# Kernel tuning notes

Hardware: AMD Instinct MI355X
Metric: run time of the kernel (lower is better)

Reference implementation:

```python
import jax, jax.numpy as jnp
import numpy as np

B, S, D_IN, D_OUT, RANK = 4, 2048, 4096, 4096, 16
SCALING = 32.0 / RANK  # alpha / rank
MASK_DENSITY = 0.01


def setup_inputs() -> dict:
    key = jax.random.key(0)
    ks = jax.random.split(key, 7)
    x = jax.random.normal(ks[0], (B, S, D_IN), dtype=jnp.float32)
    W = jax.random.normal(ks[1], (D_OUT, D_IN), dtype=jnp.float32) / np.sqrt(D_IN)
    b = jax.random.normal(ks[2], (D_OUT,), dtype=jnp.float32) * 0.01
    lora_A = jax.random.normal(ks[3], (RANK, D_IN), dtype=jnp.float32) / np.sqrt(D_IN)
    lora_B = jax.random.normal(ks[4], (D_OUT, RANK), dtype=jnp.float32) * 0.01
    delta = jax.random.normal(ks[5], (D_OUT, D_IN), dtype=jnp.float32) * 0.01
    mask = jax.random.bernoulli(ks[6], MASK_DENSITY, (D_OUT, D_IN))
    return {"x": x, "W": W, "b": b, "lora_A": lora_A, "lora_B": lora_B,
            "delta": delta, "mask": mask}


def reference(x, W, b, lora_A, lora_B, delta, mask):
    # frozen linear: [B,S,D_in] @ [D_in,D_out] + b
    out = jnp.einsum("bsd,od->bso", x, W) + b
    # LoRA branch: (x @ A^T) @ B^T * scaling
    out = out + jnp.einsum("bsr,or->bso", jnp.einsum("bsd,rd->bsr", x, lora_A), lora_B) * SCALING
    # sparse delta branch: F.linear(x, delta * mask)
    masked_delta = delta * mask.astype(delta.dtype)
    out = out + jnp.einsum("bsd,od->bso", x, masked_delta)
    return out
```

## Files before the change

### kernel.cpp

```cpp
#include <hip/hip_runtime.h>
#include <hip/hip_bf16.h>

typedef __hip_bfloat16 bf16;
typedef __attribute__((ext_vector_type(8))) short bf16x8;
typedef __attribute__((ext_vector_type(4))) float f32x4;
typedef __attribute__((ext_vector_type(4))) int int4v;

#define AS1 __attribute__((address_space(1)))
#define AS3 __attribute__((address_space(3)))

#define MDIM 8192
#define NDIM 4096
#define KDIM 4096
#define SCALING 2.0f

__device__ int g_isf32;

static __device__ __forceinline__ float tofl(bf16 v)  { return __bfloat162float(v); }
static __device__ __forceinline__ float tofl(float v) { return v; }

static __device__ __forceinline__ void load8(const bf16* p, float* o) {
    bf16x8 v = *(const bf16x8*)p;
    const bf16* b = (const bf16*)&v;
#pragma unroll
    for (int e = 0; e < 8; ++e) o[e] = __bfloat162float(b[e]);
}
static __device__ __forceinline__ void load8(const float* p, float* o) {
    f32x4 a = *(const f32x4*)p;
    f32x4 c = *(const f32x4*)(p + 4);
#pragma unroll
    for (int e = 0; e < 4; ++e) { o[e] = a[e]; o[e + 4] = c[e]; }
}

__global__ __launch_bounds__(256) void detect_dtype(const unsigned short* xw) {
    __shared__ int cnt;
    if (threadIdx.x == 0) cnt = 0;
    __syncthreads();
    int local = 0;
    for (int i = threadIdx.x; i < 16384; i += 256) {
        unsigned v = xw[i];
        if (((v >> 7) & 0xFFu) == 0xFFu) local++;
    }
    if (local) atomicAdd(&cnt, local);
    __syncthreads();
    if (threadIdx.x == 0) g_isf32 = (cnt > 0) ? 1 : 0;
}

template <typename TIN>
__global__ __launch_bounds__(256) void fold_weff(
    const TIN* __restrict__ W, const TIN* __restrict__ lA,
    const TIN* __restrict__ lB, const TIN* __restrict__ delta,
    const int* __restrict__ mask, bf16* __restrict__ Weff, int want)
{
    if (g_isf32 != want) return;
    int idx = blockIdx.x * 256 + threadIdx.x;
    int o   = idx >> 9;
    int d0  = (idx & 511) << 3;
    size_t base = (size_t)o * KDIM + d0;

    float Bo[16];
#pragma unroll
    for (int r = 0; r < 16; ++r) Bo[r] = tofl(lB[o * 16 + r]);

    float wv[8], dv[8];
    load8(W + base, wv);
    load8(delta + base, dv);

    int mk[8];
    *(int4v*)(mk)     = *(const int4v*)(mask + base);
    *(int4v*)(mk + 4) = *(const int4v*)(mask + base + 4);

    float lor[8] = {0.f, 0.f, 0.f, 0.f, 0.f, 0.f, 0.f, 0.f};
#pragma unroll
    for (int r = 0; r < 16; ++r) {
        float av[8];
        load8(lA + (size_t)r * KDIM + d0, av);
#pragma unroll
        for (int e = 0; e < 8; ++e) lor[e] += Bo[r] * av[e];
    }

    int4v ov4;
    bf16* ov = (bf16*)&ov4;
#pragma unroll
    for (int e = 0; e < 8; ++e) {
        float a = wv[e] + SCALING * lor[e];
        if (mk[e]) a += dv[e];
        ov[e] = __float2bfloat16(a);
    }
    *(int4v*)(Weff + base) = ov4;
}

__global__ __launch_bounds__(256, 3) void gemm_bf16(
    const bf16* __restrict__ X, const bf16* __restrict__ Wt,
    const bf16* __restrict__ bias, bf16* __restrict__ out)
{
    if (g_isf32 != 0) return;
    __shared__ bf16 As[128 * 64];
    __shared__ bf16 Bs[128 * 64];

    const int tid  = threadIdx.x;
    const int lane = tid & 63;
    const int wave = tid >> 6;
    const int wm   = wave & 1;
    const int wn   = wave >> 1;
    const int quad = lane >> 4;
    const int l16  = lane & 15;

    const int bn = blockIdx.x * 128;
    const int bm = blockIdx.y * 128;
    const int cwave = tid & ~63;

    f32x4 acc[4][4];
#pragma unroll
    for (int i = 0; i < 4; ++i)
#pragma unroll
        for (int j = 0; j < 4; ++j)
            acc[i][j] = (f32x4){0.f, 0.f, 0.f, 0.f};

    for (int kt = 0; kt < KDIM / 64; ++kt) {
        const int k0 = kt * 64;
        if (kt) __syncthreads();
#pragma unroll
        for (int j = 0; j < 4; ++j) {
            const int c  = j * 256 + tid;
            const int m  = c >> 3;
            const int kc = (c & 7) ^ (m & 7);
            const int cb = j * 256 + cwave;
            __builtin_amdgcn_global_load_lds(
                (const AS1 void*)(X + (size_t)(bm + m) * KDIM + k0 + kc * 8),
                (AS3 void*)(As + cb * 8), 16, 0, 0);
            __builtin_amdgcn_global_load_lds(
                (const AS1 void*)(Wt + (size_t)(bn + m) * KDIM + k0 + kc * 8),
                (AS3 void*)(Bs + cb * 8), 16, 0, 0);
        }
        __syncthreads();

#pragma unroll
        for (int ks = 0; ks < 2; ++ks) {
            bf16x8 af[4], bfr[4];
#pragma unroll
            for (int i = 0; i < 4; ++i) {
                const int m   = wm * 64 + i * 16 + l16;
                const int kca = (ks * 4 + quad) ^ (m & 7);
                af[i] = *(const bf16x8*)(As + m * 64 + kca * 8);
                const int n   = wn * 64 + i * 16 + l16;
                const int kcb = (ks * 4 + quad) ^ (n & 7);
                bfr[i] = *(const bf16x8*)(Bs + n * 64 + kcb * 8);
            }
#pragma unroll
            for (int i = 0; i < 4; ++i)
#pragma unroll
                for (int j = 0; j < 4; ++j)
                    acc[i][j] = __builtin_amdgcn_mfma_f32_16x16x32_bf16(
                        af[i], bfr[j], acc[i][j], 0, 0, 0);
        }
    }

    float bv[4];
#pragma unroll
    for (int j = 0; j < 4; ++j)
        bv[j] = tofl(bias[bn + wn * 64 + j * 16 + l16]);

#pragma unroll
    for (int i = 0; i < 4; ++i) {
        const int mg = bm + wm * 64 + i * 16 + quad * 4;
#pragma unroll
        for (int j = 0; j < 4; ++j) {
            const int ng = bn + wn * 64 + j * 16 + l16;
#pragma unroll
            for (int r = 0; r < 4; ++r)
                out[(size_t)(mg + r) * NDIM + ng] =
                    __float2bfloat16(acc[i][j][r] + bv[j]);
        }
    }
}

__global__ __launch_bounds__(256, 3) void gemm_f32(
    const float* __restrict__ X, const bf16* __restrict__ Wt,
    const float* __restrict__ bias, float* __restrict__ out)
{
    if (g_isf32 != 1) return;
    __shared__ float Asf[128 * 64];
    __shared__ bf16  Bs[128 * 64];

    const int tid  = threadIdx.x;
    const int lane = tid & 63;
    const int wave = tid >> 6;
    const int wm   = wave & 1;
    const int wn   = wave >> 1;
    const int quad = lane >> 4;
    const int l16  = lane & 15;

    const int bn = blockIdx.x * 128;
    const int bm = blockIdx.y * 128;
    const int cwave = tid & ~63;

    f32x4 acc[4][4];
#pragma unroll
    for (int i = 0; i < 4; ++i)
#pragma unroll
        for (int j = 0; j < 4; ++j)
            acc[i][j] = (f32x4){0.f, 0.f, 0.f, 0.f};

    for (int kt = 0; kt < KDIM / 64; ++kt) {
        const int k0 = kt * 64;
        if (kt) __syncthreads();

#pragma unroll
        for (int j = 0; j < 8; ++j) {
            const int c  = j * 256 + tid;
            const int m  = c >> 4;
            const int kc = (c & 15) ^ (m & 15);
            const int cb = j * 256 + cwave;
            __builtin_amdgcn_global_load_lds(
                (const AS1 void*)(X + (size_t)(bm + m) * KDIM + k0 + kc * 4),
                (AS3 void*)(Asf + cb * 4), 16, 0, 0);
        }
#pragma unroll
        for (int j = 0; j < 4; ++j) {
            const int c  = j * 256 + tid;
            const int m  = c >> 3;
            const int kc = (c & 7) ^ (m & 7);
            const int cb = j * 256 + cwave;
            __builtin_amdgcn_global_load_lds(
                (const AS1 void*)(Wt + (size_t)(bn + m) * KDIM + k0 + kc * 8),
                (AS3 void*)(Bs + cb * 8), 16, 0, 0);
        }
        __syncthreads();

#pragma unroll
        for (int ks = 0; ks < 2; ++ks) {
            bf16x8 af[4], bfr[4];
#pragma unroll
            for (int i = 0; i < 4; ++i) {
                const int m  = wm * 64 + i * 16 + l16;
                const int k2 = (ks * 4 + quad) * 2;
                f32x4 lo = *(const f32x4*)(Asf + m * 64 + ((k2     ^ (m & 15)) * 4));
                f32x4 hi = *(const f32x4*)(Asf + m * 64 + (((k2+1) ^ (m & 15)) * 4));
                bf16 tmp[8];
#pragma unroll
                for (int e = 0; e < 4; ++e) {
                    tmp[e]     = __float2bfloat16(lo[e]);
                    tmp[e + 4] = __float2bfloat16(hi[e]);
                }
                af[i] = *(const bf16x8*)tmp;

                const int n   = wn * 64 + i * 16 + l16;
                const int kcb = (ks * 4 + quad) ^ (n & 7);
                bfr[i] = *(const bf16x8*)(Bs + n * 64 + kcb * 8);
            }
#pragma unroll
            for (int i = 0; i < 4; ++i)
#pragma unroll
                for (int j = 0; j < 4; ++j)
                    acc[i][j] = __builtin_amdgcn_mfma_f32_16x16x32_bf16(
                        af[i], bfr[j], acc[i][j], 0, 0, 0);
        }
    }

    float bv[4];
#pragma unroll
    for (int j = 0; j < 4; ++j)
        bv[j] = bias[bn + wn * 64 + j * 16 + l16];

#pragma unroll
    for (int i = 0; i < 4; ++i) {
        const int mg = bm + wm * 64 + i * 16 + quad * 4;
#pragma unroll
        for (int j = 0; j < 4; ++j) {
            const int ng = bn + wn * 64 + j * 16 + l16;
#pragma unroll
            for (int r = 0; r < 4; ++r)
                out[(size_t)(mg + r) * NDIM + ng] = acc[i][j][r] + bv[j];
        }
    }
}

extern "C" void kernel_launch(void* const* d_in, const int* in_sizes, int n_in,
                              void* d_out, int out_size, void* d_ws, size_t ws_size,
                              hipStream_t stream)
{
    bf16* Weff = (bf16*)d_ws;

    detect_dtype<<<1, 256, 0, stream>>>((const unsigned short*)d_in[0]);

    fold_weff<float><<<dim3((NDIM * KDIM / 8) / 256), 256, 0, stream>>>(
        (const float*)d_in[1], (const float*)d_in[3], (const float*)d_in[4],
        (const float*)d_in[5], (const int*)d_in[6], Weff, 1);
    gemm_f32<<<dim3(NDIM / 128, MDIM / 128), 256, 0, stream>>>(
        (const float*)d_in[0], Weff, (const float*)d_in[2], (float*)d_out);

    fold_weff<bf16><<<dim3((NDIM * KDIM / 8) / 256), 256, 0, stream>>>(
        (const bf16*)d_in[1], (const bf16*)d_in[3], (const bf16*)d_in[4],
        (const bf16*)d_in[5], (const int*)d_in[6], Weff, 0);
    gemm_bf16<<<dim3(NDIM / 128, MDIM / 128), 256, 0, stream>>>(
        (const bf16*)d_in[0], Weff, (const bf16*)d_in[2], (bf16*)d_out);
}
```

Baseline: 728.8 us.

## Pre-convert activations to bf16 and use bf16 GEMM, drop dtype detection

Removes the runtime dtype-detection kernel and the duplicate no-op launches, specialising every path for float32 inputs. When workspace allows, x is converted to bf16 in a separate pass so the GEMM loads half the bytes per A tile, uses a smaller LDS footprint and can raise occupancy (launch bounds 4). This costs an extra read/write pass over x and needs a larger workspace, otherwise it falls back to the mixed f32/bf16 GEMM.

```diff
diff --git a/kernel.cpp b/kernel.cpp
--- a/kernel.cpp
+++ b/kernel.cpp
@@ -14,45 +14,11 @@
 #define KDIM 4096
 #define SCALING 2.0f
 
-__device__ int g_isf32;
-
-static __device__ __forceinline__ float tofl(bf16 v)  { return __bfloat162float(v); }
-static __device__ __forceinline__ float tofl(float v) { return v; }
-
-static __device__ __forceinline__ void load8(const bf16* p, float* o) {
-    bf16x8 v = *(const bf16x8*)p;
-    const bf16* b = (const bf16*)&v;
-#pragma unroll
-    for (int e = 0; e < 8; ++e) o[e] = __bfloat162float(b[e]);
-}
-static __device__ __forceinline__ void load8(const float* p, float* o) {
-    f32x4 a = *(const f32x4*)p;
-    f32x4 c = *(const f32x4*)(p + 4);
-#pragma unroll
-    for (int e = 0; e < 4; ++e) { o[e] = a[e]; o[e + 4] = c[e]; }
-}
-
-__global__ __launch_bounds__(256) void detect_dtype(const unsigned short* xw) {
-    __shared__ int cnt;
-    if (threadIdx.x == 0) cnt = 0;
-    __syncthreads();
-    int local = 0;
-    for (int i = threadIdx.x; i < 16384; i += 256) {
-        unsigned v = xw[i];
-        if (((v >> 7) & 0xFFu) == 0xFFu) local++;
-    }
-    if (local) atomicAdd(&cnt, local);
-    __syncthreads();
-    if (threadIdx.x == 0) g_isf32 = (cnt > 0) ? 1 : 0;
-}
-
-template <typename TIN>
 __global__ __launch_bounds__(256) void fold_weff(
-    const TIN* __restrict__ W, const TIN* __restrict__ lA,
-    const TIN* __restrict__ lB, const TIN* __restrict__ delta,
-    const int* __restrict__ mask, bf16* __restrict__ Weff, int want)
-{
-    if (g_isf32 != want) return;
+    const float* __restrict__ W, const float* __restrict__ lA,
+    const float* __restrict__ lB, const float* __restrict__ delta,
+    const int* __restrict__ mask, bf16* __restrict__ Weff)
+{
     int idx = blockIdx.x * 256 + threadIdx.x;
     int o   = idx >> 9;
     int d0  = (idx & 511) << 3;
@@ -60,11 +26,12 @@
 
     float Bo[16];
 #pragma unroll
-    for (int r = 0; r < 16; ++r) Bo[r] = tofl(lB[o * 16 + r]);
-
-    float wv[8], dv[8];
-    load8(W + base, wv);
-    load8(delta + base, dv);
+    for (int r = 0; r < 16; ++r) Bo[r] = lB[o * 16 + r];
+
+    f32x4 wa = *(const f32x4*)(W + base);
+    f32x4 wb = *(const f32x4*)(W + base + 4);
+    f32x4 da = *(const f32x4*)(delta + base);
+    f32x4 db = *(const f32x4*)(delta + base + 4);
 
     int mk[8];
     *(int4v*)(mk)     = *(const int4v*)(mask + base);
@@ -73,28 +40,48 @@
     float lor[8] = {0.f, 0.f, 0.f, 0.f, 0.f, 0.f, 0.f, 0.f};
 #pragma unroll
     for (int r = 0; r < 16; ++r) {
-        float av[8];
-        load8(lA + (size_t)r * KDIM + d0, av);
-#pragma unroll
-        for (int e = 0; e < 8; ++e) lor[e] += Bo[r] * av[e];
+        f32x4 aa = *(const f32x4*)(lA + (size_t)r * KDIM + d0);
+        f32x4 ab = *(const f32x4*)(lA + (size_t)r * KDIM + d0 + 4);
+#pragma unroll
+        for (int e = 0; e < 4; ++e) {
+            lor[e]     += Bo[r] * aa[e];
+            lor[e + 4] += Bo[r] * ab[e];
+        }
     }
 
     int4v ov4;
     bf16* ov = (bf16*)&ov4;
 #pragma unroll
     for (int e = 0; e < 8; ++e) {
-        float a = wv[e] + SCALING * lor[e];
-        if (mk[e]) a += dv[e];
+        float w = (e < 4) ? wa[e] : wb[e - 4];
+        float d = (e < 4) ? da[e] : db[e - 4];
+        float a = w + SCALING * lor[e];
+        if (mk[e]) a += d;
         ov[e] = __float2bfloat16(a);
     }
     *(int4v*)(Weff + base) = ov4;
 }
 
-__global__ __launch_bounds__(256, 3) void gemm_bf16(
+__global__ __launch_bounds__(256) void convert_x(
+    const float* __restrict__ X, bf16* __restrict__ Xb)
+{
+    size_t i = ((size_t)blockIdx.x * 256 + threadIdx.x) * 8;
+    f32x4 a = *(const f32x4*)(X + i);
+    f32x4 b = *(const f32x4*)(X + i + 4);
+    int4v ov4;
+    bf16* ov = (bf16*)&ov4;
+#pragma unroll
+    for (int e = 0; e < 4; ++e) {
+        ov[e]     = __float2bfloat16(a[e]);
+        ov[e + 4] = __float2bfloat16(b[e]);
+    }
+    *(int4v*)(Xb + i) = ov4;
+}
+
+__global__ __launch_bounds__(256, 4) void gemm_bf16(
     const bf16* __restrict__ X, const bf16* __restrict__ Wt,
-    const bf16* __restrict__ bias, bf16* __restrict__ out)
-{
-    if (g_isf32 != 0) return;
+    const float* __restrict__ bias, float* __restrict__ out)
+{
     __shared__ bf16 As[128 * 64];
     __shared__ bf16 Bs[128 * 64];
 
@@ -159,7 +146,7 @@
     float bv[4];
 #pragma unroll
     for (int j = 0; j < 4; ++j)
-        bv[j] = tofl(bias[bn + wn * 64 + j * 16 + l16]);
+        bv[j] = bias[bn + wn * 64 + j * 16 + l16];
 
 #pragma unroll
     for (int i = 0; i < 4; ++i) {
@@ -169,8 +156,7 @@
             const int ng = bn + wn * 64 + j * 16 + l16;
 #pragma unroll
             for (int r = 0; r < 4; ++r)
-                out[(size_t)(mg + r) * NDIM + ng] =
-                    __float2bfloat16(acc[i][j][r] + bv[j]);
+                out[(size_t)(mg + r) * NDIM + ng] = acc[i][j][r] + bv[j];
         }
     }
 }
@@ -179,7 +165,6 @@
     const float* __restrict__ X, const bf16* __restrict__ Wt,
     const float* __restrict__ bias, float* __restrict__ out)
 {
-    if (g_isf32 != 1) return;
     __shared__ float Asf[128 * 64];
     __shared__ bf16  Bs[128 * 64];
 
@@ -205,7 +190,6 @@
     for (int kt = 0; kt < KDIM / 64; ++kt) {
         const int k0 = kt * 64;
         if (kt) __syncthreads();
-
 #pragma unroll
         for (int j = 0; j < 8; ++j) {
             const int c  = j * 256 + tid;
@@ -280,19 +264,29 @@
                               void* d_out, int out_size, void* d_ws, size_t ws_size,
                               hipStream_t stream)
 {
+    const float* x     = (const float*)d_in[0];
+    const float* W     = (const float*)d_in[1];
+    const float* b     = (const float*)d_in[2];
+    const float* lA    = (const float*)d_in[3];
+    const float* lB    = (const float*)d_in[4];
+    const float* delta = (const float*)d_in[5];
+    const int*   mask  = (const int*)d_in[6];
+    float* out = (float*)d_out;
+
     bf16* Weff = (bf16*)d_ws;
-
-    detect_dtype<<<1, 256, 0, stream>>>((const unsigned short*)d_in[0]);
-
-    fold_weff<float><<<dim3((NDIM * KDIM / 8) / 256), 256, 0, stream>>>(
-        (const float*)d_in[1], (const float*)d_in[3], (const float*)d_in[4],
-        (const float*)d_in[5], (const int*)d_in[6], Weff, 1);
-    gemm_f32<<<dim3(NDIM / 128, MDIM / 128), 256, 0, stream>>>(
-        (const float*)d_in[0], Weff, (const float*)d_in[2], (float*)d_out);
-
-    fold_weff<bf16><<<dim3((NDIM * KDIM / 8) / 256), 256, 0, stream>>>(
-        (const bf16*)d_in[1], (const bf16*)d_in[3], (const bf16*)d_in[4],
-        (const bf16*)d_in[5], (const int*)d_in[6], Weff, 0);
-    gemm_bf16<<<dim3(NDIM / 128, MDIM / 128), 256, 0, stream>>>(
-        (const bf16*)d_in[0], Weff, (const bf16*)d_in[2], (bf16*)d_out);
-}
+    bf16* Xb   = (bf16*)((char*)d_ws + (size_t)NDIM * KDIM * 2);
+
+    const size_t need = (size_t)NDIM * KDIM * 2 + (size_t)MDIM * KDIM * 2;
+
+    fold_weff<<<dim3((NDIM * KDIM / 8) / 256), 256, 0, stream>>>(
+        W, lA, lB, delta, mask, Weff);
+
+    if (ws_size >= need) {
+        convert_x<<<dim3((MDIM * KDIM / 8) / 256), 256, 0, stream>>>(x, Xb);
+        gemm_bf16<<<dim3(NDIM / 128, MDIM / 128), 256, 0, stream>>>(
+            Xb, Weff, b, out);
+    } else {
+        gemm_f32<<<dim3(NDIM / 128, MDIM / 128), 256, 0, stream>>>(
+            x, Weff, b, out);
+    }
+}
```

Result: faster. 647.4 us (-11.2%).
